# Performance work log

Hardware: AMD Instinct MI355X
Metric: run time of the kernel (lower is better)

## Reference

```python
import jax, jax.numpy as jnp
import numpy as np

B, NB, F, N = 8192, 64, 256, 1_000_000
K = 8            # per-channel top-k
KS = K // 2 + 1  # conv1d kernel size = 5
H, OUT = 256, 128
DN = ('NWC', 'WIO', 'NWC')


def setup_inputs() -> dict:
    key = jax.random.key(0)
    ks = jax.random.split(key, 7)
    return {
        'node_ids': jax.random.randint(ks[0], (B,), 0, N, dtype=jnp.int64) if jax.config.jax_enable_x64 else jax.random.randint(ks[0], (B,), 0, N, dtype=jnp.int32),
        'neighbors': jax.random.randint(ks[1], (B, NB), 0, N, dtype=jnp.int32),
        'feat_table': jax.random.normal(ks[2], (N, F), dtype=jnp.float32),
        'W1': jax.random.normal(ks[3], (KS, F, H), dtype=jnp.float32) * 0.05,
        'b1': jnp.zeros((H,), dtype=jnp.float32),
        'W2': jax.random.normal(ks[4], (KS, H, OUT), dtype=jnp.float32) * 0.05,
        'b2': jnp.zeros((OUT,), dtype=jnp.float32),
    }


def reference(node_ids, neighbors, feat_table, W1, b1, W2, b2):
    node_feats = feat_table[node_ids][:, None, :]          # [B, 1, F]
    nb_feats = feat_table[neighbors]                       # [B, NB, F] irregular gather
    # per-channel top-k over neighbors
    topk, _ = jax.lax.top_k(jnp.transpose(nb_feats, (0, 2, 1)), K)  # [B, F, K]
    topk = jnp.transpose(topk, (0, 2, 1))                  # [B, K, F]
    x = jnp.concatenate([node_feats, topk], axis=1)        # [B, K+1, F]
    h = jax.lax.conv_general_dilated(x, W1, (1,), 'VALID', dimension_numbers=DN) + b1  # [B, K+2-KS, H]
    o = jax.lax.conv_general_dilated(h, W2, (1,), 'VALID', dimension_numbers=DN) + b2  # [B, 1, OUT]
    return o[:, 0, :]                                      # [B, OUT]
```

## Files before the change

kernel.cpp:

```cpp
#include <hip/hip_runtime.h>
#include <hip/hip_bf16.h>

namespace {
constexpr int kB    = 8192;
constexpr int kNB   = 64;
constexpr int kF    = 256;
constexpr int kK    = 8;
constexpr int kKS   = 5;
constexpr int kH    = 256;
constexpr int kOUT  = 128;
constexpr int kXR   = 9;
constexpr int kTO   = 5;
constexpr int kBM   = 16;

constexpr int XPAD = 258;
constexpr int HPAD = 1290;

constexpr size_t W1T_OFF = 0;
constexpr size_t W2T_OFF = W1T_OFF + (size_t)kKS * kH * kF * 2;

typedef __attribute__((ext_vector_type(8))) short short8;
typedef __attribute__((ext_vector_type(4))) float f32x4;
}

using bf16 = __hip_bfloat16;

__device__ __forceinline__ unsigned short f2bf(float f) {
  bf16 h = __float2bfloat16(f);
  return *reinterpret_cast<unsigned short*>(&h);
}

__global__ void convert_weights(const float* __restrict__ W1,
                                const float* __restrict__ W2,
                                bf16* __restrict__ w1t, bf16* __restrict__ w2t)
{
  const int i = blockIdx.x * 256 + threadIdx.x;
  const int stride = gridDim.x * 256;
  for (int idx = i; idx < kKS * kH * kF; idx += stride) {
    const int f  = idx & 255;
    const int hc = (idx >> 8) & 255;
    const int dt = idx >> 16;
    w1t[idx] = __float2bfloat16(W1[(dt * kF + f) * kH + hc]);
  }
  for (int idx = i; idx < kOUT * kKS * kH; idx += stride) {
    const int k = idx % (kKS * kH);
    const int o = idx / (kKS * kH);
    w2t[idx] = __float2bfloat16(W2[k * kOUT + o]);
  }
}

__global__ __launch_bounds__(256)
void fused_all(const int* __restrict__ node_ids,
               const int* __restrict__ neighbors,
               const float* __restrict__ feat,
               const bf16* __restrict__ w1t, const bf16* __restrict__ w2t,
               const float* __restrict__ b1, const float* __restrict__ b2,
               float* __restrict__ out)
{
  __shared__ bf16 smem[kBM * kXR * XPAD];
  bf16* xs = smem;
  bf16* hs = smem;

  const int tid  = threadIdx.x;
  const int wave = tid >> 6;
  const int lane = tid & 63;
  const int r = lane & 15;
  const int q = lane >> 4;
  const int bbase = blockIdx.x * kBM;
  const int f4 = lane << 2;

  int   myn4[4];
  float4 node4[4];
#pragma unroll
  for (int bb = 0; bb < 4; ++bb) {
    const int b = bbase + wave * 4 + bb;
    myn4[bb] = neighbors[(size_t)b * kNB + lane];
    node4[bb] = *reinterpret_cast<const float4*>(feat + (size_t)node_ids[b] * kF + f4);
  }

#pragma unroll
  for (int bb = 0; bb < 4; ++bb) {
    const int bl  = wave * 4 + bb;
    const int myn = myn4[bb];

    float tk[4][kK];
#pragma unroll
    for (int c = 0; c < 4; ++c)
#pragma unroll
      for (int k = 0; k < kK; ++k) tk[c][k] = -INFINITY;

    auto ins4 = [&](const float4& v) {
      const float vv[4] = {v.x, v.y, v.z, v.w};
#pragma unroll
      for (int c = 0; c < 4; ++c) {
        float nt[kK];
        nt[0] = fmaxf(tk[c][0], vv[c]);
#pragma unroll
        for (int k = 1; k < kK; ++k)
          nt[k] = __builtin_amdgcn_fmed3f(tk[c][k - 1], tk[c][k], vv[c]);
#pragma unroll
        for (int k = 0; k < kK; ++k) tk[c][k] = nt[k];
      }
    };

    float4 buf[16];
#pragma unroll
    for (int i = 0; i < 16; ++i) {
      const int rr = __builtin_amdgcn_readlane(myn, i);
      buf[i] = *reinterpret_cast<const float4*>(feat + (size_t)rr * kF + f4);
    }
#pragma unroll
    for (int g = 1; g < 4; ++g) {
#pragma unroll
      for (int i = 0; i < 16; ++i) {
        const float4 v = buf[i];
        const int rr = __builtin_amdgcn_readlane(myn, g * 16 + i);
        buf[i] = *reinterpret_cast<const float4*>(feat + (size_t)rr * kF + f4);
        ins4(v);
      }
    }
#pragma unroll
    for (int i = 0; i < 16; ++i) ins4(buf[i]);

    bf16* xb = xs + (size_t)bl * kXR * XPAD + f4;
    {
      ushort4 s = {f2bf(node4[bb].x), f2bf(node4[bb].y), f2bf(node4[bb].z), f2bf(node4[bb].w)};
      *reinterpret_cast<ushort4*>(xb) = s;
    }
#pragma unroll
    for (int k = 0; k < kK; ++k) {
      ushort4 s = {f2bf(tk[0][k]), f2bf(tk[1][k]), f2bf(tk[2][k]), f2bf(tk[3][k])};
      *reinterpret_cast<ushort4*>(xb + (size_t)(1 + k) * XPAD) = s;
    }
  }
  __syncthreads();

  const int ntb = wave * 64;
  f32x4 acc[kTO][4];
#pragma unroll
  for (int n = 0; n < 4; ++n) {
    const float bv = b1[ntb + n * 16 + r];
#pragma unroll
    for (int m = 0; m < kTO; ++m) acc[m][n] = (f32x4){bv, bv, bv, bv};
  }

  for (int kk = 0; kk < 8; ++kk) {
    short8 a[kXR];
#pragma unroll
    for (int rr = 0; rr < kXR; ++rr)
      a[rr] = *reinterpret_cast<const short8*>(&xs[(r * kXR + rr) * XPAD + kk * 32 + q * 8]);
#pragma unroll
    for (int dt = 0; dt < kKS; ++dt) {
      short8 bfr[4];
#pragma unroll
      for (int n = 0; n < 4; ++n)
        bfr[n] = *reinterpret_cast<const short8*>(
            &w1t[((size_t)(dt * kH + ntb + n * 16 + r)) * kF + kk * 32 + q * 8]);
#pragma unroll
      for (int m = 0; m < kTO; ++m)
#pragma unroll
        for (int n = 0; n < 4; ++n)
          acc[m][n] = __builtin_amdgcn_mfma_f32_16x16x32_bf16(a[m + dt], bfr[n], acc[m][n], 0, 0, 0);
    }
  }
  __syncthreads();

#pragma unroll
  for (int m = 0; m < kTO; ++m)
#pragma unroll
    for (int n = 0; n < 4; ++n)
#pragma unroll
      for (int j = 0; j < 4; ++j)
        hs[(q * 4 + j) * HPAD + m * kH + ntb + n * 16 + r] = __float2bfloat16(acc[m][n][j]);
  __syncthreads();

  const int ob = wave * 32;
  f32x4 acc2[2];
#pragma unroll
  for (int n = 0; n < 2; ++n) {
    const float bv = b2[ob + n * 16 + r];
    acc2[n] = (f32x4){bv, bv, bv, bv};
  }
  for (int ks = 0; ks < 40; ++ks) {
    short8 a2 = *reinterpret_cast<const short8*>(&hs[r * HPAD + ks * 32 + q * 8]);
#pragma unroll
    for (int n = 0; n < 2; ++n) {
      short8 b2f = *reinterpret_cast<const short8*>(
          &w2t[(size_t)(ob + n * 16 + r) * (kKS * kH) + ks * 32 + q * 8]);
      acc2[n] = __builtin_amdgcn_mfma_f32_16x16x32_bf16(a2, b2f, acc2[n], 0, 0, 0);
    }
  }
#pragma unroll
  for (int n = 0; n < 2; ++n)
#pragma unroll
    for (int j = 0; j < 4; ++j)
      out[(size_t)(bbase + q * 4 + j) * kOUT + ob + n * 16 + r] = acc2[n][j];
}

extern "C" void kernel_launch(void* const* d_in, const int* in_sizes, int n_in,
                              void* d_out, int out_size, void* d_ws, size_t ws_size,
                              hipStream_t stream) {
  const int*   node_ids  = (const int*)  d_in[0];
  const int*   neighbors = (const int*)  d_in[1];
  const float* feat      = (const float*)d_in[2];
  const float* W1        = (const float*)d_in[3];
  const float* b1        = (const float*)d_in[4];
  const float* W2        = (const float*)d_in[5];
  const float* b2        = (const float*)d_in[6];
  float* out = (float*)d_out;

  char* ws = (char*)d_ws;
  bf16* w1t = (bf16*)(ws + W1T_OFF);
  bf16* w2t = (bf16*)(ws + W2T_OFF);

  convert_weights<<<512, 256, 0, stream>>>(W1, W2, w1t, w2t);
  fused_all<<<kB / kBM, 256, 0, stream>>>(node_ids, neighbors, feat, w1t, w2t, b1, b2, out);
}
```

Measured before the change: 138.5 us.

## Use 8 waves per block and a 12-deep gather prefetch ring

Doubles the block from 4 to 8 waves. Each wave now handles 2 batch rows in the gather/top-k phase instead of 4, and the conv1 and conv2 output columns are split across twice as many waves. The neighbor gather moves from 16-deep group buffering to a rolling 12-entry prefetch ring, which cuts registers so more waves can fit on a CU and hide gather latency. The cost is less reuse of the A fragments per wave in the MFMA phases, more redundant LDS reads of xs and hs, and fewer loads in flight per wave.

```diff
diff --git a/kernel.cpp b/kernel.cpp
--- a/kernel.cpp
+++ b/kernel.cpp
@@ -16,6 +16,8 @@
 constexpr int XPAD = 258;
 constexpr int HPAD = 1290;
 
+constexpr int DEPTH = 12;
+
 constexpr size_t W1T_OFF = 0;
 constexpr size_t W2T_OFF = W1T_OFF + (size_t)kKS * kH * kF * 2;
 
@@ -49,7 +51,7 @@
   }
 }
 
-__global__ __launch_bounds__(256)
+__global__ __launch_bounds__(512, 4)
 void fused_all(const int* __restrict__ node_ids,
                const int* __restrict__ neighbors,
                const float* __restrict__ feat,
@@ -69,19 +71,19 @@
   const int bbase = blockIdx.x * kBM;
   const int f4 = lane << 2;
 
-  int   myn4[4];
-  float4 node4[4];
-#pragma unroll
-  for (int bb = 0; bb < 4; ++bb) {
-    const int b = bbase + wave * 4 + bb;
-    myn4[bb] = neighbors[(size_t)b * kNB + lane];
-    node4[bb] = *reinterpret_cast<const float4*>(feat + (size_t)node_ids[b] * kF + f4);
-  }
-
-#pragma unroll
-  for (int bb = 0; bb < 4; ++bb) {
-    const int bl  = wave * 4 + bb;
-    const int myn = myn4[bb];
+  int    myn2[2];
+  float4 node2[2];
+#pragma unroll
+  for (int bb = 0; bb < 2; ++bb) {
+    const int b = bbase + wave * 2 + bb;
+    myn2[bb]  = neighbors[(size_t)b * kNB + lane];
+    node2[bb] = *reinterpret_cast<const float4*>(feat + (size_t)node_ids[b] * kF + f4);
+  }
+
+#pragma unroll
+  for (int bb = 0; bb < 2; ++bb) {
+    const int bl  = wave * 2 + bb;
+    const int myn = myn2[bb];
 
     float tk[4][kK];
 #pragma unroll
@@ -103,28 +105,25 @@
       }
     };
 
-    float4 buf[16];
-#pragma unroll
-    for (int i = 0; i < 16; ++i) {
+    float4 buf[DEPTH];
+#pragma unroll
+    for (int i = 0; i < DEPTH; ++i) {
       const int rr = __builtin_amdgcn_readlane(myn, i);
       buf[i] = *reinterpret_cast<const float4*>(feat + (size_t)rr * kF + f4);
     }
 #pragma unroll
-    for (int g = 1; g < 4; ++g) {
-#pragma unroll
-      for (int i = 0; i < 16; ++i) {
-        const float4 v = buf[i];
-        const int rr = __builtin_amdgcn_readlane(myn, g * 16 + i);
-        buf[i] = *reinterpret_cast<const float4*>(feat + (size_t)rr * kF + f4);
-        ins4(v);
-      }
-    }
-#pragma unroll
-    for (int i = 0; i < 16; ++i) ins4(buf[i]);
+    for (int n = 0; n < kNB - DEPTH; ++n) {
+      const float4 v = buf[n % DEPTH];
+      const int rr = __builtin_amdgcn_readlane(myn, n + DEPTH);
+      buf[n % DEPTH] = *reinterpret_cast<const float4*>(feat + (size_t)rr * kF + f4);
+      ins4(v);
+    }
+#pragma unroll
+    for (int n = kNB - DEPTH; n < kNB; ++n) ins4(buf[n % DEPTH]);
 
     bf16* xb = xs + (size_t)bl * kXR * XPAD + f4;
     {
-      ushort4 s = {f2bf(node4[bb].x), f2bf(node4[bb].y), f2bf(node4[bb].z), f2bf(node4[bb].w)};
+      ushort4 s = {f2bf(node2[bb].x), f2bf(node2[bb].y), f2bf(node2[bb].z), f2bf(node2[bb].w)};
       *reinterpret_cast<ushort4*>(xb) = s;
     }
 #pragma unroll
@@ -135,10 +134,10 @@
   }
   __syncthreads();
 
-  const int ntb = wave * 64;
-  f32x4 acc[kTO][4];
-#pragma unroll
-  for (int n = 0; n < 4; ++n) {
+  const int ntb = wave * 32;
+  f32x4 acc[kTO][2];
+#pragma unroll
+  for (int n = 0; n < 2; ++n) {
     const float bv = b1[ntb + n * 16 + r];
 #pragma unroll
     for (int m = 0; m < kTO; ++m) acc[m][n] = (f32x4){bv, bv, bv, bv};
@@ -151,15 +150,15 @@
       a[rr] = *reinterpret_cast<const short8*>(&xs[(r * kXR + rr) * XPAD + kk * 32 + q * 8]);
 #pragma unroll
     for (int dt = 0; dt < kKS; ++dt) {
-      short8 bfr[4];
-#pragma unroll
-      for (int n = 0; n < 4; ++n)
+      short8 bfr[2];
+#pragma unroll
+      for (int n = 0; n < 2; ++n)
         bfr[n] = *reinterpret_cast<const short8*>(
             &w1t[((size_t)(dt * kH + ntb + n * 16 + r)) * kF + kk * 32 + q * 8]);
 #pragma unroll
       for (int m = 0; m < kTO; ++m)
 #pragma unroll
-        for (int n = 0; n < 4; ++n)
+        for (int n = 0; n < 2; ++n)
           acc[m][n] = __builtin_amdgcn_mfma_f32_16x16x32_bf16(a[m + dt], bfr[n], acc[m][n], 0, 0, 0);
     }
   }
@@ -168,33 +167,27 @@
 #pragma unroll
   for (int m = 0; m < kTO; ++m)
 #pragma unroll
-    for (int n = 0; n < 4; ++n)
+    for (int n = 0; n < 2; ++n)
 #pragma unroll
       for (int j = 0; j < 4; ++j)
         hs[(q * 4 + j) * HPAD + m * kH + ntb + n * 16 + r] = __float2bfloat16(acc[m][n][j]);
   __syncthreads();
 
-  const int ob = wave * 32;
-  f32x4 acc2[2];
-#pragma unroll
-  for (int n = 0; n < 2; ++n) {
-    const float bv = b2[ob + n * 16 + r];
-    acc2[n] = (f32x4){bv, bv, bv, bv};
+  const int ob = wave * 16;
+  f32x4 acc2;
+  {
+    const float bv = b2[ob + r];
+    acc2 = (f32x4){bv, bv, bv, bv};
   }
   for (int ks = 0; ks < 40; ++ks) {
     short8 a2 = *reinterpret_cast<const short8*>(&hs[r * HPAD + ks * 32 + q * 8]);
-#pragma unroll
-    for (int n = 0; n < 2; ++n) {
-      short8 b2f = *reinterpret_cast<const short8*>(
-          &w2t[(size_t)(ob + n * 16 + r) * (kKS * kH) + ks * 32 + q * 8]);
-      acc2[n] = __builtin_amdgcn_mfma_f32_16x16x32_bf16(a2, b2f, acc2[n], 0, 0, 0);
-    }
-  }
-#pragma unroll
-  for (int n = 0; n < 2; ++n)
-#pragma unroll
-    for (int j = 0; j < 4; ++j)
-      out[(size_t)(bbase + q * 4 + j) * kOUT + ob + n * 16 + r] = acc2[n][j];
+    short8 b2f = *reinterpret_cast<const short8*>(
+        &w2t[(size_t)(ob + r) * (kKS * kH) + ks * 32 + q * 8]);
+    acc2 = __builtin_amdgcn_mfma_f32_16x16x32_bf16(a2, b2f, acc2, 0, 0, 0);
+  }
+#pragma unroll
+  for (int j = 0; j < 4; ++j)
+    out[(size_t)(bbase + q * 4 + j) * kOUT + ob + r] = acc2[j];
 }
 
 extern "C" void kernel_launch(void* const* d_in, const int* in_sizes, int n_in,
@@ -214,5 +207,5 @@
   bf16* w2t = (bf16*)(ws + W2T_OFF);
 
   convert_weights<<<512, 256, 0, stream>>>(W1, W2, w1t, w2t);
-  fused_all<<<kB / kBM, 256, 0, stream>>>(node_ids, neighbors, feat, w1t, w2t, b1, b2, out);
-}
+  fused_all<<<kB / kBM, 512, 0, stream>>>(node_ids, neighbors, feat, w1t, w2t, b1, b2, out);
+}
```

Measured after the change: 139.5 us. About the same (+0.7%).
